# Performance work log

Measured on AMD Instinct MI355X. Metric: run time of the kernel, lower is better.

## Reference

```python
import jax, jax.numpy as jnp
from jax import lax
import numpy as np

B, N = 64, 4096


def fps(xyz, npoint):
    # Iterative farthest point sampling, deterministic start at index 0.
    # xyz: (B, N, 3) -> (B, npoint) int32 indices
    b, n, _ = xyz.shape

    def step(carry, _):
        distance, farthest = carry  # (B,N), (B,)
        centroid = jnp.take_along_axis(xyz, farthest[:, None, None], axis=1)  # (B,1,3)
        dist = jnp.sum((xyz - centroid) ** 2, axis=-1)  # (B,N)
        distance = jnp.minimum(distance, dist)
        new_far = jnp.argmax(distance, axis=-1).astype(jnp.int32)
        return (distance, new_far), farthest

    init = (jnp.full((b, n), 1e10, xyz.dtype), jnp.zeros((b,), jnp.int32))
    _, cents = lax.scan(step, init, None, length=npoint)  # (npoint, B)
    return cents.T


def gather_pts(a, idx):
    # a: (B, N, C), idx: (B, S) -> (B, S, C)
    return jnp.take_along_axis(a, idx[:, :, None], axis=1)


def setup_inputs() -> dict:
    key = jax.random.key(0)
    ks = jax.random.split(key, 16)
    s = 0.05
    return {
        'x': jax.random.normal(ks[0], (B, N, 3), jnp.float32),
        'cw1': jax.random.normal(ks[1], (3, 64), jnp.float32) * s,
        'cb1': jnp.zeros((64,), jnp.float32),
        'cw2': jax.random.normal(ks[2], (64, 1), jnp.float32) * s,
        'cb2': jnp.zeros((1,), jnp.float32),
        'w1': jax.random.normal(ks[3], (4, 64), jnp.float32) * s,
        'b1': jnp.zeros((64,), jnp.float32),
        'w2': jax.random.normal(ks[4], (64, 256), jnp.float32) * s,
        'b2': jnp.zeros((256,), jnp.float32),
        'w3': jax.random.normal(ks[5], (259, 256), jnp.float32) * s,
        'b3': jnp.zeros((256,), jnp.float32),
        'w4': jax.random.normal(ks[6], (256, 384), jnp.float32) * s,
        'b4': jnp.zeros((384,), jnp.float32),
        'w5': jax.random.normal(ks[7], (387, 384), jnp.float32) * s,
        'b5': jnp.zeros((384,), jnp.float32),
        'w6': jax.random.normal(ks[8], (384, 512), jnp.float32) * s,
        'b6': jnp.zeros((512,), jnp.float32),
        'pc1w': jax.random.normal(ks[9], (256, 256), jnp.float32) * s,
        'pc1b': jnp.zeros((256,), jnp.float32),
        'pc2w': jax.random.normal(ks[10], (384, 384), jnp.float32) * s,
        'pc2b': jnp.zeros((384,), jnp.float32),
    }


def reference(x, cw1, cb1, cw2, cb2, w1, b1, w2, b2, w3, b3, w4, b4, w5, b5, w6, b6,
              pc1w, pc1b, pc2w, pc2b):
    # ConfidenceScorePredictor (assumed per-point MLP with sigmoid output)
    conf = jax.nn.sigmoid(jax.nn.relu(x @ cw1 + cb1) @ cw2 + cb2)  # (B,N,1)
    fc = jnp.concatenate([conf, x], axis=2)                        # (B,N,4)
    l1 = jax.nn.relu(fc @ w1 + b1)                                 # (B,N,64)
    l2 = jax.nn.relu(l1 @ w2 + b2)                                 # (B,N,256)

    idx1 = fps(x, 500)
    nx1 = gather_pts(x, idx1)                                      # (B,500,3)
    nf1 = gather_pts(l2, idx1)                                     # (B,500,256)
    l3 = nf1 @ pc1w + pc1b                                         # conv1d k=1 == linear
    l4 = jax.nn.relu(jnp.concatenate([nx1, l3], axis=2) @ w3 + b3) # (B,500,256)
    l5 = jax.nn.relu(l4 @ w4 + b4)                                 # (B,500,384)

    idx2 = fps(nx1, 250)
    nx2 = gather_pts(nx1, idx2)                                    # (B,250,3)
    nf2 = gather_pts(l5, idx2)                                     # (B,250,384)
    l6 = nf2 @ pc2w + pc2b
    l7 = jax.nn.relu(jnp.concatenate([nx2, l6], axis=2) @ w5 + b5) # (B,250,384)

    # NOTE: faithful to source oddity - third FPS runs on nx2 (250 pts) but
    # gathers new_xyz from the ORIGINAL x with those indices.
    idx3 = fps(nx2, 125)
    nf3 = gather_pts(l7, idx3)                                     # (B,125,384)
    l8 = jax.nn.relu(nf3 @ w6 + b6)                                # (B,125,512)
    out = jnp.max(l8, axis=1)                                      # (B,512)
    return out, conf
```

## Files before the change

### kernel.cpp

```cpp
#include <hip/hip_runtime.h>
#include <hip/hip_bf16.h>
#include <cstdint>
#include <cstddef>

#define BB 64
#define NN 4096

typedef short bf16x8 __attribute__((ext_vector_type(8)));
typedef float f32x4 __attribute__((ext_vector_type(4)));
typedef unsigned short u16;
typedef unsigned int u32;

__device__ __forceinline__ u16 f2bf(float f) {
  __hip_bfloat16 h = __float2bfloat16(f);
  return *reinterpret_cast<u16*>(&h);
}
__device__ __forceinline__ float bf2f(u16 u) {
  return __uint_as_float((u32)u << 16);
}

__device__ __forceinline__ float sqdist(float px, float py, float pz,
                                        float cx, float cy, float cz) {
  float dx = px - cx, dy = py - cy, dz = pz - cz;
  return __fadd_rn(__fadd_rn(__fmul_rn(dx, dx), __fmul_rn(dy, dy)),
                   __fmul_rn(dz, dz));
}

__device__ __forceinline__ unsigned long long u64max(unsigned long long a,
                                                    unsigned long long b) {
  return a > b ? a : b;
}

template<int CTRL, int RM>
__device__ __forceinline__ void dpp_max_step(u32& hi, u32& lo) {
  u32 ohi = (u32)__builtin_amdgcn_update_dpp((int)hi, (int)hi, CTRL, RM, 0xf, false);
  u32 olo = (u32)__builtin_amdgcn_update_dpp((int)lo, (int)lo, CTRL, RM, 0xf, false);
  bool gt = (ohi > hi) || ((ohi == hi) && (olo > lo));
  hi = gt ? ohi : hi;
  lo = gt ? olo : lo;
}

__device__ __forceinline__ void wave_argmax_to_lane63(u32& hi, u32& lo) {
  dpp_max_step<0x111, 0xf>(hi, lo);
  dpp_max_step<0x112, 0xf>(hi, lo);
  dpp_max_step<0x114, 0xf>(hi, lo);
  dpp_max_step<0x118, 0xf>(hi, lo);
  dpp_max_step<0x142, 0xa>(hi, lo);
  dpp_max_step<0x143, 0xc>(hi, lo);
}

template<int NPER>
__device__ void fps_wave(const float* __restrict__ xb, int n, int npoint,
                         int* __restrict__ idx_out, float* __restrict__ sel_out,
                         float* pts)
{
  const int lane = threadIdx.x;
  for (int i = lane; i < n * 3; i += 64) pts[i] = xb[i];
  for (int i = n * 3 + lane; i < NPER * 64 * 3; i += 64) pts[i] = 0.f;

  float px[NPER], py[NPER], pz[NPER], dst[NPER];
#pragma unroll
  for (int k = 0; k < NPER; ++k) {
    int i = k * 64 + lane;
    px[k] = pts[i*3+0]; py[k] = pts[i*3+1]; pz[k] = pts[i*3+2];
    dst[k] = (i < n) ? 1e10f : 0.f;
  }

  int far = 0;
  float cx = pts[0], cy = pts[1], cz = pts[2];

  for (int it = 0; it < npoint; ++it) {
    if (lane == 0) {
      idx_out[it] = far;
      if (sel_out) {
        sel_out[it*3+0] = cx; sel_out[it*3+1] = cy; sel_out[it*3+2] = cz;
      }
    }
    float bestd = -1.f; int besti = 0;
#pragma unroll
    for (int k = 0; k < NPER; ++k) {
      float nd = fminf(dst[k], sqdist(px[k], py[k], pz[k], cx, cy, cz));
      dst[k] = nd;
      if (nd > bestd) { bestd = nd; besti = k * 64 + lane; }
    }
    u32 hi = __float_as_uint(bestd);
    u32 lo = 0xFFFFFFFFu - (u32)besti;
    wave_argmax_to_lane63(hi, lo);
    far = (int)(0xFFFFFFFFu - (u32)__builtin_amdgcn_readlane((int)lo, 63));
    cx = pts[far*3+0]; cy = pts[far*3+1]; cz = pts[far*3+2];
  }
}

__global__ __launch_bounds__(256) void fps1_conf_wtx_kernel(
    const float* __restrict__ x,
    const float* __restrict__ cw1, const float* __restrict__ cb1,
    const float* __restrict__ cw2, const float* __restrict__ cb2,
    const float* __restrict__ pc1w, const float* __restrict__ w3,
    const float* __restrict__ w4,  const float* __restrict__ pc2w,
    const float* __restrict__ w5,  const float* __restrict__ w6,
    int* __restrict__ idx1, float* __restrict__ nx1,
    float* __restrict__ conf_out,
    u16* wt1, u16* wt3, u16* wt4, u16* wtp2, u16* wt5, u16* wt6)
{
  if (blockIdx.x >= BB + 1024) {
    int s = (blockIdx.x - (BB + 1024)) * 256 + threadIdx.x;
    const float* src; u16* dst; int N, Ks, Kp;
    if      (s < 8192)  { dst=wt1;  src=pc1w; N=256; Ks=256; Kp=256; }
    else if (s < 17408) { dst=wt3;  src=w3;   N=256; Ks=259; Kp=288; s -= 8192; }
    else if (s < 29696) { dst=wt4;  src=w4;   N=384; Ks=256; Kp=256; s -= 17408; }
    else if (s < 48128) { dst=wtp2; src=pc2w; N=384; Ks=384; Kp=384; s -= 29696; }
    else if (s < 68096) { dst=wt5;  src=w5;   N=384; Ks=387; Kp=416; s -= 48128; }
    else                { dst=wt6;  src=w6;   N=512; Ks=384; Kp=384; s -= 68096; }
    int e0 = s * 8;
    int n = e0 / Kp, k0 = e0 % Kp;
    u16 tmp[8];
#pragma unroll
    for (int j = 0; j < 8; ++j) {
      int k = k0 + j;
      tmp[j] = f2bf(k < Ks ? src[k*N + n] : 0.f);
    }
    *(uint4*)&dst[e0] = *(const uint4*)tmp;
    return;
  }
  if (blockIdx.x >= BB) {
    int i = (blockIdx.x - BB) * 256 + threadIdx.x;
    if (i < BB * NN) {
      float x0 = x[i*3+0], x1 = x[i*3+1], x2 = x[i*3+2];
      float acc = cb2[0];
#pragma unroll
      for (int j = 0; j < 64; ++j) {
        float h = fmaxf(x0*cw1[j] + x1*cw1[64+j] + x2*cw1[128+j] + cb1[j], 0.f);
        acc += h * cw2[j];
      }
      conf_out[i] = 1.f / (1.f + expf(-acc));
    }
    return;
  }

  constexpr int NPER = NN / 256;
  __shared__ float pts[NN * 3];
  __shared__ unsigned long long sh_pk[2][4];
  __shared__ int   idx_lds[500];
  __shared__ float nx_lds[1500];
  const int b = blockIdx.x, tid = threadIdx.x;
  const float* xb = x + (size_t)b * NN * 3;

  for (int i = tid; i < NN * 3; i += 256) pts[i] = xb[i];
  __syncthreads();

  float px[NPER], py[NPER], pz[NPER], dstv[NPER];
#pragma unroll
  for (int k = 0; k < NPER; ++k) {
    int i = k * 256 + tid;
    px[k] = pts[i*3+0]; py[k] = pts[i*3+1]; pz[k] = pts[i*3+2];
    dstv[k] = 1e10f;
  }

  int far = 0;
  float cx = pts[0], cy = pts[1], cz = pts[2];

  for (int it = 0; it < 500; ++it) {
    if (tid == 0) {
      idx_lds[it] = far;
      nx_lds[it*3+0] = cx; nx_lds[it*3+1] = cy; nx_lds[it*3+2] = cz;
    }
    float bestd = -1.f; int besti = 0;
#pragma unroll
    for (int k = 0; k < NPER; ++k) {
      int i = k * 256 + tid;
      float nd = fminf(dstv[k], sqdist(px[k], py[k], pz[k], cx, cy, cz));
      dstv[k] = nd;
      if (nd > bestd) { bestd = nd; besti = i; }
    }
    u32 hi = __float_as_uint(bestd);
    u32 lo = 0xFFFFFFFFu - (u32)besti;
    wave_argmax_to_lane63(hi, lo);
    if ((tid & 63) == 63)
      sh_pk[it & 1][tid >> 6] = ((unsigned long long)hi << 32) | lo;
    __syncthreads();
    unsigned long long m = u64max(u64max(sh_pk[it&1][0], sh_pk[it&1][1]),
                                  u64max(sh_pk[it&1][2], sh_pk[it&1][3]));
    far = (int)(0xFFFFFFFFu - (u32)(m & 0xFFFFFFFFull));
    cx = pts[far*3+0]; cy = pts[far*3+1]; cz = pts[far*3+2];
  }

  __syncthreads();
  for (int i = tid; i < 500; i += 256)  idx1[b*500 + i] = idx_lds[i];
  for (int i = tid; i < 1500; i += 256) nx1[(size_t)b*1500 + i] = nx_lds[i];
}

__global__ __launch_bounds__(256) void fps2_selfeat_cat1fix_kernel(
    const float* __restrict__ x, const float* __restrict__ nx1,
    const int* __restrict__ idx1,
    const float* __restrict__ cw1, const float* __restrict__ cb1,
    const float* __restrict__ cw2, const float* __restrict__ cb2,
    const float* __restrict__ w1, const float* __restrict__ b1,
    const float* __restrict__ w2, const float* __restrict__ b2,
    int* __restrict__ idx2, float* __restrict__ nx2,
    u16* __restrict__ nf1, u16* __restrict__ cat1)
{
  __shared__ float pts[8 * 64 * 3];
  __shared__ float l1s[4][64];

  if (blockIdx.x < BB) {
    if (threadIdx.x >= 64) return;
    int b = blockIdx.x;
    fps_wave<8>(nx1 + (size_t)b*500*3, 500, 250,
                idx2 + b*250, nx2 + (size_t)b*250*3, pts);
    return;
  }
  if (blockIdx.x >= BB + 8000) {
    int r = (blockIdx.x - (BB + 8000)) * 256 + threadIdx.x;
    u16* row = cat1 + (size_t)r * 288;
    row[0] = f2bf(nx1[r*3+0]);
    row[1] = f2bf(nx1[r*3+1]);
    row[2] = f2bf(nx1[r*3+2]);
#pragma unroll
    for (int c = 259; c < 288; ++c) row[c] = 0;
    return;
  }

  int wid  = threadIdx.x >> 6;
  int lane = threadIdx.x & 63;
  int gw   = (blockIdx.x - BB) * 4 + wid;
  int b = gw / 500, s = gw % 500;
  int p = idx1[b*500 + s];
  const float* xp = x + ((size_t)b * NN + p) * 3;
  float x0 = xp[0], x1 = xp[1], x2 = xp[2];

  float h = fmaxf(x0*cw1[lane] + x1*cw1[64+lane] + x2*cw1[128+lane] + cb1[lane], 0.f);
  float part = h * cw2[lane];
#pragma unroll
  for (int o = 32; o > 0; o >>= 1) part += __shfl_xor(part, o);
  float conf = 1.f / (1.f + expf(-(part + cb2[0])));

  float l1v = fmaxf(conf*w1[lane] + x0*w1[64+lane] + x1*w1[128+lane]
                    + x2*w1[192+lane] + b1[lane], 0.f);
  l1s[wid][lane] = l1v;
  __syncthreads();

  float a0 = b2[lane], a1 = b2[64+lane], a2 = b2[128+lane], a3 = b2[192+lane];
#pragma unroll
  for (int k = 0; k < 64; ++k) {
    float lv = l1s[wid][k];
    const float* wr = w2 + k*256;
    a0 += lv * wr[lane];
    a1 += lv * wr[64+lane];
    a2 += lv * wr[128+lane];
    a3 += lv * wr[192+lane];
  }
  u16* o = nf1 + (size_t)gw * 256;
  o[lane]     = f2bf(fmaxf(a0, 0.f));
  o[64+lane]  = f2bf(fmaxf(a1, 0.f));
  o[128+lane] = f2bf(fmaxf(a2, 0.f));
  o[192+lane] = f2bf(fmaxf(a3, 0.f));
}

__device__ __forceinline__ void mfma_gemm_body(
    const u16* __restrict__ A, const u16* __restrict__ Wt,
    const float* __restrict__ bias, u16* __restrict__ C,
    int K, int ldc, int act, int bx, int by,
    u16 (*As)[40], u16 (*Bs)[40])
{
  const int tid = threadIdx.x;
  const int wid = tid >> 6, lane = tid & 63;
  const int lr = lane & 15, lg = lane >> 4;
  const int brow = by * 64, bcol = bx * 128;

  f32x4 acc[4][2] = {};

  const int ar = tid >> 2, ac = (tid & 3) * 8;
  const u16* Arow  = A  + (size_t)(brow + ar) * K + ac;
  const u16* Brow0 = Wt + (size_t)(bcol + ar) * K + ac;
  const u16* Brow1 = Wt + (size_t)(bcol + 64 + ar) * K + ac;

  for (int k0 = 0; k0 < K; k0 += 32) {
    uint4 va  = *(const uint4*)(Arow  + k0);
    uint4 vb0 = *(const uint4*)(Brow0 + k0);
    uint4 vb1 = *(const uint4*)(Brow1 + k0);
    *(uint4*)&As[ar][ac]      = va;
    *(uint4*)&Bs[ar][ac]      = vb0;
    *(uint4*)&Bs[64 + ar][ac] = vb1;
    __syncthreads();

    bf16x8 af[4], bfr[2];
#pragma unroll
    for (int i = 0; i < 4; ++i)
      af[i] = *(const bf16x8*)&As[i*16 + lr][lg*8];
#pragma unroll
    for (int j = 0; j < 2; ++j)
      bfr[j] = *(const bf16x8*)&Bs[wid*32 + j*16 + lr][lg*8];
#pragma unroll
    for (int i = 0; i < 4; ++i)
#pragma unroll
      for (int j = 0; j < 2; ++j)
        acc[i][j] = __builtin_amdgcn_mfma_f32_16x16x32_bf16(
            af[i], bfr[j], acc[i][j], 0, 0, 0);
    __syncthreads();
  }

#pragma unroll
  for (int i = 0; i < 4; ++i) {
#pragma unroll
    for (int j = 0; j < 2; ++j) {
      int col = bcol + wid*32 + j*16 + lr;
      float bv = bias[col];
#pragma unroll
      for (int r = 0; r < 4; ++r) {
        int row = brow + i*16 + lg*4 + r;
        float v = acc[i][j][r] + bv;
        if (act) v = fmaxf(v, 0.f);
        C[(size_t)row * ldc + col] = f2bf(v);
      }
    }
  }
}

__global__ __launch_bounds__(256) void gemm_kernel(
    const u16* __restrict__ A, const u16* __restrict__ Wt,
    const float* __restrict__ bias, u16* __restrict__ C,
    int K, int Nc, int ldc, int act)
{
  __shared__ __align__(16) u16 As[64][40];
  __shared__ __align__(16) u16 Bs[128][40];
  int nbx = Nc >> 7;
  mfma_gemm_body(A, Wt, bias, C, K, ldc, act,
                 blockIdx.x % nbx, blockIdx.x / nbx, As, Bs);
}

__global__ __launch_bounds__(256) void fps3_gemm_kernel(
    const float* __restrict__ nx2, int* __restrict__ idx3,
    const u16* __restrict__ A, const u16* __restrict__ Wt,
    const float* __restrict__ bias, u16* __restrict__ C,
    int K, int Nc, int ldc, int act)
{
  __shared__ __align__(16) u16 As[64][40];
  __shared__ __align__(16) u16 Bs[128][40];
  __shared__ float pts[4 * 64 * 3];
  if (blockIdx.x < BB) {
    if (threadIdx.x >= 64) return;
    fps_wave<4>(nx2 + (size_t)blockIdx.x*250*3, 250, 125,
                idx3 + blockIdx.x*125, nullptr, pts);
    return;
  }
  int blk = blockIdx.x - BB;
  int nbx = Nc >> 7;
  mfma_gemm_body(A, Wt, bias, C, K, ldc, act, blk % nbx, blk / nbx, As, Bs);
}

__global__ __launch_bounds__(256) void gatherb_cat2fix_kernel(
    const u16* __restrict__ src, const int* __restrict__ idx,
    u16* __restrict__ dst, int Ss, int Sd, int C, int gather_blocks,
    const float* __restrict__ nx2, u16* __restrict__ cat2, int rows)
{
  if ((int)blockIdx.x >= gather_blocks) {
    int r = ((int)blockIdx.x - gather_blocks) * 256 + threadIdx.x;
    if (r < rows) {
      u16* row = cat2 + (size_t)r * 416;
      row[0] = f2bf(nx2[r*3+0]);
      row[1] = f2bf(nx2[r*3+1]);
      row[2] = f2bf(nx2[r*3+2]);
#pragma unroll
      for (int c = 387; c < 416; ++c) row[c] = 0;
    }
    return;
  }
  int i = blockIdx.x * 256 + threadIdx.x;
  int C8 = C >> 3;
  int total = BB * Sd * C8;
  if (i >= total) return;
  int c = i % C8, t = i / C8, s = t % Sd, b = t / Sd;
  int p = idx[b*Sd + s];
  *(uint4*)&dst[(size_t)i * 8] =
      *(const uint4*)&src[(size_t)(b*Ss + p) * C + c*8];
}

__global__ __launch_bounds__(256) void gatherb_kernel(
    const u16* __restrict__ src, const int* __restrict__ idx,
    u16* __restrict__ dst, int Ss, int Sd, int C)
{
  int i = blockIdx.x * 256 + threadIdx.x;
  int C8 = C >> 3;
  int total = BB * Sd * C8;
  if (i >= total) return;
  int c = i % C8, t = i / C8, s = t % Sd, b = t / Sd;
  int p = idx[b*Sd + s];
  *(uint4*)&dst[(size_t)i * 8] =
      *(const uint4*)&src[(size_t)(b*Ss + p) * C + c*8];
}

__global__ __launch_bounds__(256) void maxpool_kernel(
    const u16* __restrict__ l8, float* __restrict__ out)
{
  int i = blockIdx.x * 256 + threadIdx.x;
  if (i >= BB * 512) return;
  int b = i >> 9, n = i & 511;
  const u16* p = l8 + (size_t)b * 125 * 512 + n;
  float m = bf2f(p[0]);
  for (int s = 1; s < 125; ++s) m = fmaxf(m, bf2f(p[(size_t)s * 512]));
  out[i] = m;
}

extern "C" void kernel_launch(void* const* d_in, const int* in_sizes, int n_in,
                              void* d_out, int out_size, void* d_ws, size_t ws_size,
                              hipStream_t stream)
{
  const float* x    = (const float*)d_in[0];
  const float* cw1  = (const float*)d_in[1];
  const float* cb1  = (const float*)d_in[2];
  const float* cw2  = (const float*)d_in[3];
  const float* cb2  = (const float*)d_in[4];
  const float* w1   = (const float*)d_in[5];
  const float* b1   = (const float*)d_in[6];
  const float* w2   = (const float*)d_in[7];
  const float* b2   = (const float*)d_in[8];
  const float* w3   = (const float*)d_in[9];
  const float* b3   = (const float*)d_in[10];
  const float* w4   = (const float*)d_in[11];
  const float* b4   = (const float*)d_in[12];
  const float* w5   = (const float*)d_in[13];
  const float* b5   = (const float*)d_in[14];
  const float* w6   = (const float*)d_in[15];
  const float* b6   = (const float*)d_in[16];
  const float* pc1w = (const float*)d_in[17];
  const float* pc1b = (const float*)d_in[18];
  const float* pc2w = (const float*)d_in[19];
  const float* pc2b = (const float*)d_in[20];

  float* out      = (float*)d_out;
  float* conf_out = out + 64*512;

  char* ws = (char*)d_ws;
  size_t off = 0;
  auto alloc = [&](size_t bytes) -> void* {
    void* p = ws + off;
    off = (off + bytes + 255) & ~(size_t)255;
    return p;
  };
  int*   idx1 = (int*)alloc((size_t)BB*500*4);
  int*   idx2 = (int*)alloc((size_t)BB*250*4);
  int*   idx3 = (int*)alloc((size_t)BB*125*4);
  float* nx1  = (float*)alloc((size_t)BB*500*3*4);
  float* nx2  = (float*)alloc((size_t)BB*250*3*4);
  u16* wt1  = (u16*)alloc((size_t)256*256*2);
  u16* wt3  = (u16*)alloc((size_t)256*288*2);
  u16* wt4  = (u16*)alloc((size_t)384*256*2);
  u16* wtp2 = (u16*)alloc((size_t)384*384*2);
  u16* wt5  = (u16*)alloc((size_t)384*416*2);
  u16* wt6  = (u16*)alloc((size_t)512*384*2);
  u16* P1 = (u16*)alloc((size_t)32000*256*2);
  u16* P2 = (u16*)alloc((size_t)32000*288*2);
  u16* P3 = (u16*)alloc((size_t)32000*384*2);
  (void)ws_size; (void)in_sizes; (void)n_in; (void)out_size;

  fps1_conf_wtx_kernel<<<BB + 1024 + 362, 256, 0, stream>>>(
      x, cw1, cb1, cw2, cb2, pc1w, w3, w4, pc2w, w5, w6,
      idx1, nx1, conf_out, wt1, wt3, wt4, wtp2, wt5, wt6);

  fps2_selfeat_cat1fix_kernel<<<BB + 8000 + 125, 256, 0, stream>>>(
      x, nx1, idx1, cw1, cb1, cw2, cb2, w1, b1, w2, b2, idx2, nx2, P1, P2);

  gemm_kernel<<<1000, 256, 0, stream>>>(P1, wt1, pc1b, P2 + 3, 256, 256, 288, 0);

  fps3_gemm_kernel<<<BB + 1000, 256, 0, stream>>>(
      nx2, idx3, P2, wt3, b3, P1, 288, 256, 256, 1);

  gemm_kernel<<<1500, 256, 0, stream>>>(P1, wt4, b4, P3, 256, 384, 384, 1);

  gatherb_cat2fix_kernel<<<3000 + 63, 256, 0, stream>>>(
      P3, idx2, P2, 500, 250, 384, 3000, nx2, P1, 16000);

  gemm_kernel<<<750, 256, 0, stream>>>(P2, wtp2, pc2b, P1 + 3, 384, 384, 416, 0);

  gemm_kernel<<<750, 256, 0, stream>>>(P1, wt5, b5, P2, 416, 384, 384, 1);

  gatherb_kernel<<<1500, 256, 0, stream>>>(P2, idx3, P3, 250, 125, 384);

  gemm_kernel<<<500, 256, 0, stream>>>(P3, wt6, b6, P1, 384, 512, 512, 1);

  maxpool_kernel<<<128, 256, 0, stream>>>(P1, out);
}
```

Baseline: 609.2 us.

## Widen FPS blocks to 1024 threads and parallelize second FPS across a block

The first farthest-point-sampling kernel now runs each batch with 1024 threads (4 points per thread instead of 16). It stores points as float4 in shared memory and replaces the serial cross-wave max with a DPP reduction over 16 wave partials. The second FPS moves from a single wave per batch to a full 256-thread block with a 4-wave DPP reduction. Together these shorten the serial per-iteration critical path, at the cost of more barrier participants and lower occupancy for the fused conf and weight-transpose side blocks.

```diff
diff --git a/kernel.cpp b/kernel.cpp
--- a/kernel.cpp
+++ b/kernel.cpp
@@ -24,11 +24,6 @@
   float dx = px - cx, dy = py - cy, dz = pz - cz;
   return __fadd_rn(__fadd_rn(__fmul_rn(dx, dx), __fmul_rn(dy, dy)),
                    __fmul_rn(dz, dz));
-}
-
-__device__ __forceinline__ unsigned long long u64max(unsigned long long a,
-                                                    unsigned long long b) {
-  return a > b ? a : b;
 }
 
 template<int CTRL, int RM>
@@ -91,7 +86,7 @@
   }
 }
 
-__global__ __launch_bounds__(256) void fps1_conf_wtx_kernel(
+__global__ __launch_bounds__(1024) void fps1_conf_wtx_kernel(
     const float* __restrict__ x,
     const float* __restrict__ cw1, const float* __restrict__ cb1,
     const float* __restrict__ cw2, const float* __restrict__ cb2,
@@ -102,8 +97,9 @@
     float* __restrict__ conf_out,
     u16* wt1, u16* wt3, u16* wt4, u16* wtp2, u16* wt5, u16* wt6)
 {
-  if (blockIdx.x >= BB + 1024) {
-    int s = (blockIdx.x - (BB + 1024)) * 256 + threadIdx.x;
+  if (blockIdx.x >= BB + 256) {
+    int s = (blockIdx.x - (BB + 256)) * 1024 + threadIdx.x;
+    if (s >= 92672) return;
     const float* src; u16* dst; int N, Ks, Kp;
     if      (s < 8192)  { dst=wt1;  src=pc1w; N=256; Ks=256; Kp=256; }
     else if (s < 17408) { dst=wt3;  src=w3;   N=256; Ks=259; Kp=288; s -= 8192; }
@@ -123,41 +119,44 @@
     return;
   }
   if (blockIdx.x >= BB) {
-    int i = (blockIdx.x - BB) * 256 + threadIdx.x;
-    if (i < BB * NN) {
-      float x0 = x[i*3+0], x1 = x[i*3+1], x2 = x[i*3+2];
-      float acc = cb2[0];
-#pragma unroll
-      for (int j = 0; j < 64; ++j) {
-        float h = fmaxf(x0*cw1[j] + x1*cw1[64+j] + x2*cw1[128+j] + cb1[j], 0.f);
-        acc += h * cw2[j];
-      }
-      conf_out[i] = 1.f / (1.f + expf(-acc));
-    }
+    int i = (blockIdx.x - BB) * 1024 + threadIdx.x;
+    float x0 = x[i*3+0], x1 = x[i*3+1], x2 = x[i*3+2];
+    float acc = cb2[0];
+#pragma unroll
+    for (int j = 0; j < 64; ++j) {
+      float h = fmaxf(x0*cw1[j] + x1*cw1[64+j] + x2*cw1[128+j] + cb1[j], 0.f);
+      acc += h * cw2[j];
+    }
+    conf_out[i] = 1.f / (1.f + expf(-acc));
     return;
   }
 
-  constexpr int NPER = NN / 256;
-  __shared__ float pts[NN * 3];
-  __shared__ unsigned long long sh_pk[2][4];
+  constexpr int T = 1024, NPER = NN / T;
+  __shared__ float4 pts4[NN];
+  __shared__ unsigned long long sh_pk[2][16];
   __shared__ int   idx_lds[500];
   __shared__ float nx_lds[1500];
   const int b = blockIdx.x, tid = threadIdx.x;
+  const int lane = tid & 63, wv = tid >> 6;
   const float* xb = x + (size_t)b * NN * 3;
 
-  for (int i = tid; i < NN * 3; i += 256) pts[i] = xb[i];
+  for (int i = tid; i < NN; i += T) {
+    const float* p = xb + i*3;
+    pts4[i] = make_float4(p[0], p[1], p[2], 0.f);
+  }
   __syncthreads();
 
   float px[NPER], py[NPER], pz[NPER], dstv[NPER];
 #pragma unroll
   for (int k = 0; k < NPER; ++k) {
-    int i = k * 256 + tid;
-    px[k] = pts[i*3+0]; py[k] = pts[i*3+1]; pz[k] = pts[i*3+2];
+    float4 c = pts4[k*T + tid];
+    px[k] = c.x; py[k] = c.y; pz[k] = c.z;
     dstv[k] = 1e10f;
   }
 
   int far = 0;
-  float cx = pts[0], cy = pts[1], cz = pts[2];
+  float4 c0 = pts4[0];
+  float cx = c0.x, cy = c0.y, cz = c0.z;
 
   for (int it = 0; it < 500; ++it) {
     if (tid == 0) {
@@ -167,7 +166,7 @@
     float bestd = -1.f; int besti = 0;
 #pragma unroll
     for (int k = 0; k < NPER; ++k) {
-      int i = k * 256 + tid;
+      int i = k * T + tid;
       float nd = fminf(dstv[k], sqdist(px[k], py[k], pz[k], cx, cy, cz));
       dstv[k] = nd;
       if (nd > bestd) { bestd = nd; besti = i; }
@@ -175,18 +174,23 @@
     u32 hi = __float_as_uint(bestd);
     u32 lo = 0xFFFFFFFFu - (u32)besti;
     wave_argmax_to_lane63(hi, lo);
-    if ((tid & 63) == 63)
-      sh_pk[it & 1][tid >> 6] = ((unsigned long long)hi << 32) | lo;
+    if (lane == 63)
+      sh_pk[it & 1][wv] = ((unsigned long long)hi << 32) | lo;
     __syncthreads();
-    unsigned long long m = u64max(u64max(sh_pk[it&1][0], sh_pk[it&1][1]),
-                                  u64max(sh_pk[it&1][2], sh_pk[it&1][3]));
-    far = (int)(0xFFFFFFFFu - (u32)(m & 0xFFFFFFFFull));
-    cx = pts[far*3+0]; cy = pts[far*3+1]; cz = pts[far*3+2];
+    unsigned long long v = sh_pk[it & 1][lane & 15];
+    u32 chi = (u32)(v >> 32), clo = (u32)v;
+    dpp_max_step<0x111, 0xf>(chi, clo);
+    dpp_max_step<0x112, 0xf>(chi, clo);
+    dpp_max_step<0x114, 0xf>(chi, clo);
+    dpp_max_step<0x118, 0xf>(chi, clo);
+    far = (int)(0xFFFFFFFFu - (u32)__builtin_amdgcn_readlane((int)clo, 15));
+    float4 cc = pts4[far];
+    cx = cc.x; cy = cc.y; cz = cc.z;
   }
 
   __syncthreads();
-  for (int i = tid; i < 500; i += 256)  idx1[b*500 + i] = idx_lds[i];
-  for (int i = tid; i < 1500; i += 256) nx1[(size_t)b*1500 + i] = nx_lds[i];
+  for (int i = tid; i < 500; i += T)  idx1[b*500 + i] = idx_lds[i];
+  for (int i = tid; i < 1500; i += T) nx1[(size_t)b*1500 + i] = nx_lds[i];
 }
 
 __global__ __launch_bounds__(256) void fps2_selfeat_cat1fix_kernel(
@@ -199,18 +203,72 @@
     int* __restrict__ idx2, float* __restrict__ nx2,
     u16* __restrict__ nf1, u16* __restrict__ cat1)
 {
-  __shared__ float pts[8 * 64 * 3];
+  __shared__ float4 q4[512];
+  __shared__ unsigned long long spk[2][4];
+  __shared__ int   i2_lds[250];
+  __shared__ float n2_lds[750];
   __shared__ float l1s[4][64];
 
+  const int tid = threadIdx.x;
+
   if (blockIdx.x < BB) {
-    if (threadIdx.x >= 64) return;
-    int b = blockIdx.x;
-    fps_wave<8>(nx1 + (size_t)b*500*3, 500, 250,
-                idx2 + b*250, nx2 + (size_t)b*250*3, pts);
+    const int lane = tid & 63, wv = tid >> 6;
+    const int b = blockIdx.x;
+    const float* nb = nx1 + (size_t)b * 500 * 3;
+    for (int i = tid; i < 500; i += 256)
+      q4[i] = make_float4(nb[i*3+0], nb[i*3+1], nb[i*3+2], 0.f);
+    for (int i = 500 + tid; i < 512; i += 256)
+      q4[i] = make_float4(0.f, 0.f, 0.f, 0.f);
+    __syncthreads();
+
+    float px[2], py[2], pz[2], ds[2];
+#pragma unroll
+    for (int k = 0; k < 2; ++k) {
+      int i = k * 256 + tid;
+      float4 c = q4[i];
+      px[k] = c.x; py[k] = c.y; pz[k] = c.z;
+      ds[k] = (i < 500) ? 1e10f : 0.f;
+    }
+
+    int far = 0;
+    float4 c0 = q4[0];
+    float cx = c0.x, cy = c0.y, cz = c0.z;
+
+    for (int it = 0; it < 250; ++it) {
+      if (tid == 0) {
+        i2_lds[it] = far;
+        n2_lds[it*3+0] = cx; n2_lds[it*3+1] = cy; n2_lds[it*3+2] = cz;
+      }
+      float bestd = -1.f; int besti = 0;
+#pragma unroll
+      for (int k = 0; k < 2; ++k) {
+        float nd = fminf(ds[k], sqdist(px[k], py[k], pz[k], cx, cy, cz));
+        ds[k] = nd;
+        if (nd > bestd) { bestd = nd; besti = k * 256 + tid; }
+      }
+      u32 hi = __float_as_uint(bestd);
+      u32 lo = 0xFFFFFFFFu - (u32)besti;
+      wave_argmax_to_lane63(hi, lo);
+      if (lane == 63)
+        spk[it & 1][wv] = ((unsigned long long)hi << 32) | lo;
+      __syncthreads();
+      unsigned long long v = spk[it & 1][lane & 3];
+      u32 chi = (u32)(v >> 32), clo = (u32)v;
+      dpp_max_step<0x111, 0xf>(chi, clo);
+      dpp_max_step<0x112, 0xf>(chi, clo);
+      far = (int)(0xFFFFFFFFu - (u32)__builtin_amdgcn_readlane((int)clo, 3));
+      float4 cc = q4[far];
+      cx = cc.x; cy = cc.y; cz = cc.z;
+    }
+
+    __syncthreads();
+    for (int i = tid; i < 250; i += 256) idx2[blockIdx.x*250 + i] = i2_lds[i];
+    for (int i = tid; i < 750; i += 256)
+      nx2[(size_t)blockIdx.x*750 + i] = n2_lds[i];
     return;
   }
   if (blockIdx.x >= BB + 8000) {
-    int r = (blockIdx.x - (BB + 8000)) * 256 + threadIdx.x;
+    int r = (blockIdx.x - (BB + 8000)) * 256 + tid;
     u16* row = cat1 + (size_t)r * 288;
     row[0] = f2bf(nx1[r*3+0]);
     row[1] = f2bf(nx1[r*3+1]);
@@ -220,8 +278,8 @@
     return;
   }
 
-  int wid  = threadIdx.x >> 6;
-  int lane = threadIdx.x & 63;
+  int wid  = tid >> 6;
+  int lane = tid & 63;
   int gw   = (blockIdx.x - BB) * 4 + wid;
   int b = gw / 500, s = gw % 500;
   int p = idx1[b*500 + s];
@@ -453,7 +511,7 @@
   u16* P3 = (u16*)alloc((size_t)32000*384*2);
   (void)ws_size; (void)in_sizes; (void)n_in; (void)out_size;
 
-  fps1_conf_wtx_kernel<<<BB + 1024 + 362, 256, 0, stream>>>(
+  fps1_conf_wtx_kernel<<<BB + 256 + 91, 1024, 0, stream>>>(
       x, cw1, cb1, cw2, cb2, pc1w, w3, w4, pc2w, w5, w6,
       idx1, nx1, conf_out, wt1, wt3, wt4, wtp2, wt5, wt6);
 
```

New measurement: 769.1 us. 26.3% more time.
